# Kernel tuning notes

Measured on AMD Instinct MI355X. Metric: run time of the kernel, lower is better.

## Reference

```python
import jax, jax.numpy as jnp
import numpy as np
import math

B, S, D, H, DFF = 4, 1024, 1024, 16, 4096
DK = D // H
EPS = 1e-5


def setup_inputs() -> dict:
    key = jax.random.key(0)
    ks = jax.random.split(key, 20)
    n = lambda k, shp: jax.random.normal(k, shp, jnp.float32) * 0.02
    inp = {
        "x": jax.random.normal(ks[0], (B, S, D), jnp.float32),
        "enc_output": jax.random.normal(ks[1], (B, S, D), jnp.float32),
        # source_mask is unused by the module's forward; target_mask is causal
        "source_mask": jnp.ones((B, 1, 1, S), jnp.int32),
        "target_mask": jnp.tril(jnp.ones((1, 1, S, S), jnp.int32)),
        # self-attention (torch Linear: y = x @ W.T + b)
        "sa_wq": n(ks[2], (D, D)), "sa_bq": jnp.zeros((D,), jnp.float32),
        "sa_wk": n(ks[3], (D, D)), "sa_bk": jnp.zeros((D,), jnp.float32),
        "sa_wv": n(ks[4], (D, D)), "sa_bv": jnp.zeros((D,), jnp.float32),
        "sa_wo": n(ks[5], (D, D)), "sa_bo": jnp.zeros((D,), jnp.float32),
        # cross-attention (nn.MultiheadAttention packed in_proj)
        "ca_in_w": n(ks[6], (3 * D, D)), "ca_in_b": jnp.zeros((3 * D,), jnp.float32),
        "ca_out_w": n(ks[7], (D, D)), "ca_out_b": jnp.zeros((D,), jnp.float32),
        # feed-forward
        "ff_w1": n(ks[8], (DFF, D)), "ff_b1": jnp.zeros((DFF,), jnp.float32),
        "ff_w2": n(ks[9], (D, DFF)), "ff_b2": jnp.zeros((D,), jnp.float32),
        # layer norms
        "n1_g": jnp.ones((D,), jnp.float32), "n1_b": jnp.zeros((D,), jnp.float32),
        "n2_g": jnp.ones((D,), jnp.float32), "n2_b": jnp.zeros((D,), jnp.float32),
        "n3_g": jnp.ones((D,), jnp.float32), "n3_b": jnp.zeros((D,), jnp.float32),
    }
    return inp


def _layernorm(x, g, b):
    m = jnp.mean(x, axis=-1, keepdims=True)
    v = jnp.var(x, axis=-1, keepdims=True)
    return (x - m) * jax.lax.rsqrt(v + EPS) * g + b


def _split_heads(t):  # [B,L,D] -> [B,H,L,DK]
    Bb, L, _ = t.shape
    return t.reshape(Bb, L, H, DK).transpose(0, 2, 1, 3)


def _attn(q, k, v, mask):
    # q,k,v: [B,H,Lq/ Lk, DK]
    scores = jnp.einsum("bhqd,bhkd->bhqk", q, k) / math.sqrt(DK)
    if mask is not None:
        scores = jnp.where(mask == 0, jnp.float32(-1e9), scores)
    probs = jax.nn.softmax(scores, axis=-1)
    out = jnp.einsum("bhqk,bhkd->bhqd", probs, v)  # [B,H,Lq,DK]
    Bb, _, Lq, _ = out.shape
    return out.transpose(0, 2, 1, 3).reshape(Bb, Lq, D)


def reference(x, enc_output, source_mask, target_mask,
              sa_wq, sa_bq, sa_wk, sa_bk, sa_wv, sa_bv, sa_wo, sa_bo,
              ca_in_w, ca_in_b, ca_out_w, ca_out_b,
              ff_w1, ff_b1, ff_w2, ff_b2,
              n1_g, n1_b, n2_g, n2_b, n3_g, n3_b):
    # --- masked causal self-attention (hand-rolled MultiHeadAttention) ---
    q = _split_heads(x @ sa_wq.T + sa_bq)
    k = _split_heads(x @ sa_wk.T + sa_bk)
    v = _split_heads(x @ sa_wv.T + sa_bv)
    sa = _attn(q, k, v, target_mask) @ sa_wo.T + sa_bo
    x = _layernorm(x + sa, n1_g, n1_b)  # dropout p=0 -> identity

    # --- cross-attention (nn.MultiheadAttention, batch_first, no mask) ---
    wq, wk, wv = ca_in_w[:D], ca_in_w[D:2 * D], ca_in_w[2 * D:]
    bq, bk, bv = ca_in_b[:D], ca_in_b[D:2 * D], ca_in_b[2 * D:]
    q = _split_heads(x @ wq.T + bq)
    k = _split_heads(enc_output @ wk.T + bk)
    v = _split_heads(enc_output @ wv.T + bv)
    ca = _attn(q, k, v, None) @ ca_out_w.T + ca_out_b
    x = _layernorm(x + ca, n2_g, n2_b)

    # --- feed-forward ---
    ff = jax.nn.relu(x @ ff_w1.T + ff_b1) @ ff_w2.T + ff_b2
    x = _layernorm(x + ff, n3_g, n3_b)
    return x
```

## Files before the change

### kernel.cpp

```cpp
#include <hip/hip_runtime.h>
#include <hip/hip_bf16.h>
#include <stdint.h>
#include <math.h>

#define DEV static __device__ __forceinline__

typedef short bf16x8 __attribute__((ext_vector_type(8)));
typedef float f32x4 __attribute__((ext_vector_type(4)));
typedef float f32x16 __attribute__((ext_vector_type(16)));
typedef unsigned short u16;

static constexpr int Sq   = 1024;
static constexpr int Dm   = 1024;
static constexpr int Hh   = 16;
static constexpr int Mrows = 4096;
static constexpr int DFFn = 4096;


DEV u16 f2bf(float f) {
    union { float f; unsigned u; } c; c.f = f;
    unsigned u = c.u;
    return (u16)((u + 0x7FFFu + ((u >> 16) & 1u)) >> 16);
}

DEV float bf2f(u16 v) {
    union { unsigned u; float f; } c; c.u = ((unsigned)v) << 16; return c.f;
}

DEV unsigned cvt_pk_bf16(float lo, float hi) {
    unsigned r;
    asm("v_cvt_pk_bf16_f32 %0, %1, %2" : "=v"(r) : "v"(lo), "v"(hi));
    return r;
}

DEV float fast_exp2(float x) {
#if __has_builtin(__builtin_amdgcn_exp2f)
    return __builtin_amdgcn_exp2f(x);
#else
    float r; asm("v_exp_f32 %0, %1" : "=v"(r) : "v"(x)); return r;
#endif
}

DEV void gload_lds16(void* lds, const void* g) {
    using gvp = __attribute__((address_space(1))) void*;
    using lvp = __attribute__((address_space(3))) void*;
    __builtin_amdgcn_global_load_lds((gvp)const_cast<void*>(g), (lvp)lds, 16, 0, 0);
}

DEV int swz64(int L) { return L ^ (((L >> 7) & 7) << 4); }


__global__ __launch_bounds__(256) void cast_multi_kernel(
    const float* s0, const float* s1, const float* s2, const float* s3, const float* s4,
    const float* s5, const float* s6, const float* s7, const float* s8, const float* s9,
    u16* d0, u16* d1, u16* d2, u16* d3, u16* d4,
    u16* d5, u16* d6, u16* d7, u16* d8, u16* d9,
    int e0, int e1, int e2, int e3, int e4,
    int e5, int e6, int e7, int e8, int e9)
{
    int i = blockIdx.x * 256 + threadIdx.x;
    if (i >= e9) return;
    const float* s; u16* d; int b;
    if      (i < e0) { s = s0; d = d0; b = 0;  }
    else if (i < e1) { s = s1; d = d1; b = e0; }
    else if (i < e2) { s = s2; d = d2; b = e1; }
    else if (i < e3) { s = s3; d = d3; b = e2; }
    else if (i < e4) { s = s4; d = d4; b = e3; }
    else if (i < e5) { s = s5; d = d5; b = e4; }
    else if (i < e6) { s = s6; d = d6; b = e5; }
    else if (i < e7) { s = s7; d = d7; b = e6; }
    else if (i < e8) { s = s8; d = d8; b = e7; }
    else             { s = s9; d = d9; b = e8; }
    int j = i - b;
    float4 v = ((const float4*)s)[j];
    ushort4 o;
    o.x = f2bf(v.x); o.y = f2bf(v.y); o.z = f2bf(v.z); o.w = f2bf(v.w);
    ((ushort4*)d)[j] = o;
}


template<int MODE, int BSPLIT>
__global__ __launch_bounds__(512) void gemm256_kernel(
    const u16* __restrict__ A, const u16* __restrict__ W,
    const float* __restrict__ bias0, const float* __restrict__ bias1,
    const float* __restrict__ bias2,
    void* __restrict__ Cout,
    void* __restrict__ P1, void* __restrict__ P2, void* __restrict__ P3,
    int N, int ldK, int Kpass)
{
    __shared__ char ldsA[65536];
    __shared__ char ldsB[65536];
    const int tid = threadIdx.x;
    const int w = tid >> 6, l = tid & 63;
    const int lr = l & 15, lg = l >> 4;
    const int wr = w >> 2, wc = w & 3;

    const int nwg = gridDim.x * gridDim.y;
    const int lin = blockIdx.y * gridDim.x + blockIdx.x;
    const int swz = (lin & 7) * (nwg >> 3) + (lin >> 3);
    const size_t tm = (size_t)(swz / gridDim.x) * 256;
    const size_t tn = (size_t)(swz % gridDim.x) * 256;
    const size_t kz = (size_t)blockIdx.z * Kpass;

    int offA[8], offB[4];
    #pragma unroll
    for (int m = 0; m < 8; ++m)
        offA[m] = swz64((wr * 128 + m * 16 + lr) * 64 + lg * 16);
    #pragma unroll
    for (int n = 0; n < 4; ++n)
        offB[n] = swz64((wc * 64 + n * 16 + lr) * 64 + lg * 16);

    const int Ls = swz64(tid * 16);
    const int sr = Ls >> 6, scc = Ls & 63;
    const size_t ldb = (size_t)ldK * 2;
    const char* aS = (const char*)A + (tm + sr) * ldb + kz * 2 + scc;
    const char* bS = (const char*)W + (tn + sr) * ldb + kz * 2 + scc;

    auto AH = [&](int b, int h) -> char* { return ldsA + (b * 2 + h) * 16384; };
    auto BH = [&](int b, int h) -> char* { return ldsB + (b * 2 + h) * 16384; };
    auto stage = [&](char* half, const char* src) {
        gload_lds16(half + w * 1024, src);
        gload_lds16(half + 8192 + w * 1024, src + 128 * ldb);
    };

    const int nt = Kpass >> 6;
    const int niter = nt >> 1;

    f32x4 acc[8][4] = {};
    bf16x8 bq[4];

    stage(AH(0, 0), aS);        stage(BH(0, 0), bS);
    stage(AH(0, 1), aS + 64);   stage(BH(0, 1), bS + 64);
    stage(AH(1, 0), aS + 128);  stage(BH(1, 0), bS + 128);
    asm volatile("s_waitcnt vmcnt(4)" ::: "memory");
    __builtin_amdgcn_s_barrier();

    for (int it = 0; it < niter; ++it) {
        const int t0 = it * 2;
        const bool last = (it == niter - 1);
        #pragma unroll
        for (int p = 0; p < 8; ++p) {
            const int ts = p >> 2;
            const int kk = (p >> 1) & 1, mh = p & 1;

            if (mh == 0) {
                #pragma unroll
                for (int n = 0; n < 4; ++n)
                    bq[n] = *(const bf16x8*)(BH(ts, kk) + offB[n]);
            }
            bf16x8 aF[4];
            #pragma unroll
            for (int q = 0; q < 4; ++q)
                aF[q] = *(const bf16x8*)(AH(ts, kk) + offA[mh * 4 + q]);

            if (p == 0)      { stage(AH(1, 1), aS + (size_t)(t0 + 1) * 128 + 64); }
            else if (p == 1) { stage(BH(1, 1), bS + (size_t)(t0 + 1) * 128 + 64); }
            else if (p == 2) { if (t0 + 2 < nt) stage(AH(0, 0), aS + (size_t)(t0 + 2) * 128); }
            else if (p == 3) { if (t0 + 2 < nt) stage(BH(0, 0), bS + (size_t)(t0 + 2) * 128); }
            else if (p == 4) { if (t0 + 2 < nt) stage(AH(0, 1), aS + (size_t)(t0 + 2) * 128 + 64); }
            else if (p == 5) { if (t0 + 2 < nt) stage(BH(0, 1), bS + (size_t)(t0 + 2) * 128 + 64); }
            else if (p == 6) { if (t0 + 3 < nt) stage(AH(1, 0), aS + (size_t)(t0 + 3) * 128); }
            else             { if (t0 + 3 < nt) stage(BH(1, 0), bS + (size_t)(t0 + 3) * 128); }

            if (p == 3) {
                if (last) asm volatile("s_waitcnt vmcnt(0)" ::: "memory");
                else      asm volatile("s_waitcnt vmcnt(4)" ::: "memory");
            } else if (p == 7 && !last) {
                asm volatile("s_waitcnt vmcnt(4)" ::: "memory");
            }
            __builtin_amdgcn_s_barrier();
            asm volatile("s_waitcnt lgkmcnt(0)");
            __builtin_amdgcn_sched_barrier(0);
            __builtin_amdgcn_s_setprio(1);
            #pragma unroll
            for (int q = 0; q < 4; ++q)
                #pragma unroll
                for (int n = 0; n < 4; ++n)
                    acc[mh * 4 + q][n] = __builtin_amdgcn_mfma_f32_16x16x32_bf16(
                        aF[q], bq[n], acc[mh * 4 + q][n], 0, 0, 0);
            __builtin_amdgcn_s_setprio(0);
            __builtin_amdgcn_s_barrier();
        }
    }

    u16* Pp = nullptr;
    float bv[4];
    if (MODE == 3) {
        Pp = (u16*)((blockIdx.z == 0) ? Cout : (blockIdx.z == 1) ? P1 : (blockIdx.z == 2) ? P2 : P3);
    } else {
        #pragma unroll
        for (int n = 0; n < 4; ++n) {
            const int col = (int)tn + wc * 64 + n * 16 + lr;
            if (BSPLIT) {
                const float* bp = (col < 1024) ? bias0 : (col < 2048) ? bias1 : bias2;
                bv[n] = bp[col & 1023];
            } else {
                bv[n] = bias0[col];
            }
        }
    }
    #pragma unroll
    for (int m = 0; m < 8; ++m) {
        #pragma unroll
        for (int n = 0; n < 4; ++n) {
            const size_t col = tn + wc * 64 + n * 16 + lr;
            #pragma unroll
            for (int j = 0; j < 4; ++j) {
                const size_t row = tm + wr * 128 + m * 16 + lg * 4 + j;
                if (MODE == 3) {
                    Pp[row * (size_t)N + col] = f2bf(acc[m][n][j]);
                } else {
                    float v = acc[m][n][j] + bv[n];
                    if (MODE == 2) v = fmaxf(v, 0.f);
                    ((u16*)Cout)[row * (size_t)N + col] = f2bf(v);
                }
            }
        }
    }
}


template<int OUT_BF16, int RELU>
__global__ __launch_bounds__(256) void gemm_bt64_kernel(
    const u16* __restrict__ A, const u16* __restrict__ W,
    const float* __restrict__ bias, void* __restrict__ Cout,
    int N, int K)
{
    __shared__ char Ald[64 * 64];
    __shared__ char Bld[128 * 64];
    const int tid = threadIdx.x;
    const int w  = tid >> 6, l = tid & 63;
    const int lr = l & 15,  lg = l >> 4;

    const int nwg = gridDim.x * gridDim.y;
    const int lin = blockIdx.y * gridDim.x + blockIdx.x;
    const int swz = (lin & 7) * (nwg >> 3) + (lin >> 3);
    const size_t tm = (size_t)(swz / gridDim.x) * 64;
    const size_t tn = (size_t)(swz % gridDim.x) * 128;

    const int Ls = swz64(tid * 16);
    const int sr = Ls >> 6, scc = Ls & 63;
    const u16* Asrc = A + (tm + sr) * (size_t)K + (scc >> 1);
    const u16* Bsrc = W + (tn + sr) * (size_t)K + (scc >> 1);
    char* AldW = Ald + w * 1024;
    char* BldW = Bld + w * 1024;

    f32x4 acc[4][2] = {};

    for (int k0 = 0; k0 < K; k0 += 32) {
        __syncthreads();
        gload_lds16(AldW,        Asrc + k0);
        gload_lds16(BldW,        Bsrc + k0);
        gload_lds16(BldW + 4096, Bsrc + (size_t)64 * K + k0);
        __syncthreads();

        bf16x8 af[4], bfv[2];
        #pragma unroll
        for (int m = 0; m < 4; ++m)
            af[m] = *(const bf16x8*)(Ald + swz64((m * 16 + lr) * 64 + lg * 16));
        #pragma unroll
        for (int n = 0; n < 2; ++n)
            bfv[n] = *(const bf16x8*)(Bld + swz64((w * 32 + n * 16 + lr) * 64 + lg * 16));
        #pragma unroll
        for (int m = 0; m < 4; ++m)
            #pragma unroll
            for (int n = 0; n < 2; ++n)
                acc[m][n] = __builtin_amdgcn_mfma_f32_16x16x32_bf16(af[m], bfv[n], acc[m][n], 0, 0, 0);
    }

    float bv[2];
    #pragma unroll
    for (int n = 0; n < 2; ++n) bv[n] = bias[tn + w * 32 + n * 16 + lr];

    #pragma unroll
    for (int m = 0; m < 4; ++m) {
        #pragma unroll
        for (int n = 0; n < 2; ++n) {
            const size_t col = tn + w * 32 + n * 16 + lr;
            #pragma unroll
            for (int j = 0; j < 4; ++j) {
                const size_t row = tm + m * 16 + lg * 4 + j;
                float v = acc[m][n][j] + bv[n];
                if (RELU) v = fmaxf(v, 0.f);
                if (OUT_BF16) ((u16*)Cout)[row * (size_t)N + col] = f2bf(v);
                else          ((float*)Cout)[row * (size_t)N + col] = v;
            }
        }
    }
}


template<int CAUSAL>
__global__ __launch_bounds__(512, 2) void attn_kernel(
    const u16* __restrict__ Qm, int ldq,
    const u16* __restrict__ Km, int ldk,
    const u16* __restrict__ Vm, int ldv,
    u16* __restrict__ Om)
{
    __shared__ char lds[33280];

    const int tid = threadIdx.x;
    const int w = tid >> 6, l = tid & 63;
    const int lq = l & 31, hi = l >> 5;
    const int s = w & 3, hfk = w >> 2;
    const int bh = blockIdx.x;
    const int b = bh >> 4, h = bh & 15;
    const int q0 = (CAUSAL ? (gridDim.y - 1 - blockIdx.y) : blockIdx.y) * 128;
    const int qw0 = q0 + s * 32;
    const size_t baseQ = (size_t)b * Sq * ldq + (size_t)h * 64;
    const size_t baseK = (size_t)b * Sq * ldk + (size_t)h * 64;
    const size_t baseV = (size_t)b * Sq * ldv + (size_t)h * 64;
    const size_t baseO = (size_t)b * Sq * Dm  + (size_t)h * 64;

    const int qrow = qw0 + lq;
    bf16x8 bq[4];
    #pragma unroll
    for (int kc = 0; kc < 4; ++kc)
        bq[kc] = *(const bf16x8*)&Qm[baseQ + (size_t)qrow * ldq + kc * 16 + hi * 8];

    const int tl = tid & 255, pstg = tid >> 8;
    const int kr  = tl >> 2;
    const int kcB = (tl & 3) * 32;
    const int vdg = tl >> 5;
    const int vkp = tl & 31;
    char* Kst = lds + pstg * 8192;
    char* Vst = lds + 16384 + pstg * 8192;
    const char* Kb_ = lds + hfk * 8192;
    const char* Vb_ = lds + 16384 + hfk * 8192;

    f32x16 o0 = {}, o1 = {};
    float lj = 0.f;

    const int nt_blk  = CAUSAL ? ((q0 + 128) >> 6) : (Sq >> 6);
    const int nrounds = nt_blk >> 1;
    const float cexp = 0.125f * 1.44269504f;
    const float CSH  = 10.0f;

    uint4 kaA, kbA, vaA, vbA, kaB, kbB, vaB, vbB;
    auto loadKV = [&](int rv, uint4& ka, uint4& kb, uint4& va, uint4& vb) {
        const int kv = (rv * 2 + pstg) << 6;
        ka = *(const uint4*)&Km[baseK + (size_t)(kv + kr) * ldk + kcB / 2];
        kb = *(const uint4*)&Km[baseK + (size_t)(kv + kr) * ldk + kcB / 2 + 8];
        va = *(const uint4*)&Vm[baseV + (size_t)(kv + vkp * 2    ) * ldv + vdg * 8];
        vb = *(const uint4*)&Vm[baseV + (size_t)(kv + vkp * 2 + 1) * ldv + vdg * 8];
    };

    loadKV(0, kaA, kbA, vaA, vbA);
    if (nrounds > 1) loadKV(1, kaB, kbB, vaB, vbB);

    for (int r = 0; r < nrounds; ++r) {
        {
            const int sk = (kr & 7) << 4;
            *(uint4*)(Kst + kr * 128 + ((kcB     ) ^ sk)) = kaA;
            *(uint4*)(Kst + kr * 128 + ((kcB + 16) ^ sk)) = kbA;
            const u16* pa_ = (const u16*)&vaA;
            const u16* pb_ = (const u16*)&vbA;
            #pragma unroll
            for (int i = 0; i < 8; ++i) {
                const int d = vdg * 8 + i;
                unsigned val = (unsigned)pa_[i] | ((unsigned)pb_[i] << 16);
                *(unsigned*)(Vst + d * 128 + ((vkp * 4) ^ ((d & 7) << 4))) = val;
            }
        }
        __syncthreads();
        if (r + 2 < nrounds) loadKV(r + 2, kaA, kbA, vaA, vbA);

        const int kv0 = (r * 2 + hfk) << 6;
        if (!CAUSAL || kv0 < qw0 + 32) {
            const int skq = (lq & 7) << 4;

            f32x16 sv[2] = {};
            #pragma unroll
            for (int n = 0; n < 2; ++n) {
                const int rowb = (n * 32 + lq) * 128;
                #pragma unroll
                for (int kc = 0; kc < 4; ++kc) {
                    bf16x8 kf = *(const bf16x8*)(Kb_ + rowb + ((kc * 32 + hi * 16) ^ skq));
                    sv[n] = __builtin_amdgcn_mfma_f32_32x32x16_bf16(kf, bq[kc], sv[n], 0, 0, 0);
                }
            }

            const bool diag = CAUSAL && (kv0 + 63 > qw0);
            float rs0 = 0.f, rs1 = 0.f;
            #pragma unroll
            for (int n = 0; n < 2; ++n)
                #pragma unroll
                for (int r2 = 0; r2 < 16; ++r2) {
                    float v = sv[n][r2];
                    if (diag) {
                        int key = kv0 + n * 32 + (r2 & 3) + 8 * (r2 >> 2) + 4 * hi;
                        if (key > qrow) v = -3.0e8f;
                    }
                    float e = fast_exp2(fmaf(v, cexp, -CSH));
                    sv[n][r2] = e;
                    if (r2 & 1) rs1 += e; else rs0 += e;
                }
            float rs = rs0 + rs1;
            rs += __shfl_xor(rs, 32);
            lj += rs;

            unsigned wv[2][8];
            #pragma unroll
            for (int n = 0; n < 2; ++n)
                #pragma unroll
                for (int m = 0; m < 8; ++m)
                    wv[n][m] = cvt_pk_bf16(sv[n][2 * m], sv[n][2 * m + 1]);

            #pragma unroll
            for (int ks = 0; ks < 4; ++ks) {
                const int n = ks >> 1, q_ = (ks & 1) * 4;
                unsigned r0 = (unsigned)__shfl_xor((int)wv[n][q_ + 0], 32);
                unsigned r1 = (unsigned)__shfl_xor((int)wv[n][q_ + 1], 32);
                unsigned r2w = (unsigned)__shfl_xor((int)wv[n][q_ + 2], 32);
                unsigned r3 = (unsigned)__shfl_xor((int)wv[n][q_ + 3], 32);
                union { unsigned u[4]; bf16x8 v; } pa;
                pa.u[0] = hi ? r2w          : wv[n][q_ + 0];
                pa.u[1] = hi ? r3           : wv[n][q_ + 1];
                pa.u[2] = hi ? wv[n][q_ + 2] : r0;
                pa.u[3] = hi ? wv[n][q_ + 3] : r1;
                const int koff = (ks * 32 + hi * 16);
                bf16x8 vf0 = *(const bf16x8*)(Vb_ + lq * 128        + (koff ^ skq));
                bf16x8 vf1 = *(const bf16x8*)(Vb_ + (32 + lq) * 128 + (koff ^ skq));
                o0 = __builtin_amdgcn_mfma_f32_32x32x16_bf16(pa.v, vf0, o0, 0, 0, 0);
                o1 = __builtin_amdgcn_mfma_f32_32x32x16_bf16(pa.v, vf1, o1, 0, 0, 0);
            }
        }
        __syncthreads();

        uint4 t;
        t = kaA; kaA = kaB; kaB = t;
        t = kbA; kbA = kbB; kbB = t;
        t = vaA; vaA = vaB; vaB = t;
        t = vbA; vbA = vbB; vbB = t;
    }

    char* ob = lds + s * 8192 + l * 128;
    float* mlb = (float*)(lds + 32768) + s * 32 + lq;
    const int sko = (l & 7) << 4;

    if (hfk == 1) {
        #pragma unroll
        for (int i = 0; i < 4; ++i) {
            f32x4 t0v = { o0[4 * i], o0[4 * i + 1], o0[4 * i + 2], o0[4 * i + 3] };
            f32x4 t1v = { o1[4 * i], o1[4 * i + 1], o1[4 * i + 2], o1[4 * i + 3] };
            *(f32x4*)(ob + ((i * 16) ^ sko))      = t0v;
            *(f32x4*)(ob + ((64 + i * 16) ^ sko)) = t1v;
        }
        if (hi == 0) mlb[0] = lj;
    }
    __syncthreads();
    if (hfk == 0) {
        const float linv = __builtin_amdgcn_rcpf(lj + mlb[0]);
        f32x4 b0[4], b1[4];
        #pragma unroll
        for (int i = 0; i < 4; ++i) {
            b0[i] = *(const f32x4*)(ob + ((i * 16) ^ sko));
            b1[i] = *(const f32x4*)(ob + ((64 + i * 16) ^ sko));
        }
        #pragma unroll
        for (int r2 = 0; r2 < 16; ++r2) {
            const int crow = (r2 & 3) + 8 * (r2 >> 2) + 4 * hi;
            const float lr_ = __shfl(linv, crow);
            const size_t rowoff = baseO + (size_t)(qw0 + crow) * Dm;
            float v0 = (o0[r2] + b0[r2 >> 2][r2 & 3]) * lr_;
            float v1 = (o1[r2] + b1[r2 >> 2][r2 & 3]) * lr_;
            Om[rowoff + lq]      = f2bf(v0);
            Om[rowoff + 32 + lq] = f2bf(v1);
        }
    }
}


__global__ __launch_bounds__(256) void add_ln_kernel(
    const float* __restrict__ A, const float* __restrict__ Bv,
    const float* __restrict__ g, const float* __restrict__ be,
    float* __restrict__ Y, u16* __restrict__ Ybf)
{
    const int row = blockIdx.x;
    const int tid = threadIdx.x;
    const size_t off = (size_t)row * Dm;
    float4 a4 = ((const float4*)(A + off))[tid];
    float4 b4 = ((const float4*)(Bv + off))[tid];
    float4 xv;
    xv.x = a4.x + b4.x; xv.y = a4.y + b4.y; xv.z = a4.z + b4.z; xv.w = a4.w + b4.w;
    float s = xv.x + xv.y + xv.z + xv.w;
    float q = xv.x * xv.x + xv.y * xv.y + xv.z * xv.z + xv.w * xv.w;
    #pragma unroll
    for (int m = 1; m < 64; m <<= 1) {
        s += __shfl_xor(s, m);
        q += __shfl_xor(q, m);
    }
    __shared__ float ss[4], qq[4];
    if ((tid & 63) == 0) { ss[tid >> 6] = s; qq[tid >> 6] = q; }
    __syncthreads();
    s = ss[0] + ss[1] + ss[2] + ss[3];
    q = qq[0] + qq[1] + qq[2] + qq[3];
    const float mean = s * (1.f / 1024.f);
    const float var  = q * (1.f / 1024.f) - mean * mean;
    const float rstd = rsqrtf(var + 1e-5f);
    float4 g4  = ((const float4*)g)[tid];
    float4 be4 = ((const float4*)be)[tid];
    float4 y;
    y.x = (xv.x - mean) * rstd * g4.x + be4.x;
    y.y = (xv.y - mean) * rstd * g4.y + be4.y;
    y.z = (xv.z - mean) * rstd * g4.z + be4.z;
    y.w = (xv.w - mean) * rstd * g4.w + be4.w;
    ((float4*)(Y + off))[tid] = y;
    if (Ybf) {
        ushort4 ob;
        ob.x = f2bf(y.x); ob.y = f2bf(y.y); ob.z = f2bf(y.z); ob.w = f2bf(y.w);
        ((ushort4*)(Ybf + off))[tid] = ob;
    }
}


__global__ __launch_bounds__(256) void add_ln_red4_kernel(
    const float* __restrict__ X,
    const u16* __restrict__ P0, const u16* __restrict__ P1,
    const u16* __restrict__ P2, const u16* __restrict__ P3,
    const float* __restrict__ bias,
    const float* __restrict__ g, const float* __restrict__ be,
    float* __restrict__ Y)
{
    const int row = blockIdx.x;
    const int tid = threadIdx.x;
    const size_t off = (size_t)row * Dm;
    float4 a4 = ((const float4*)(X + off))[tid];
    ushort4 u0 = ((const ushort4*)(P0 + off))[tid];
    ushort4 u1 = ((const ushort4*)(P1 + off))[tid];
    ushort4 u2 = ((const ushort4*)(P2 + off))[tid];
    ushort4 u3 = ((const ushort4*)(P3 + off))[tid];
    float4 b4 = ((const float4*)bias)[tid];
    float4 xv;
    xv.x = a4.x + bf2f(u0.x) + bf2f(u1.x) + bf2f(u2.x) + bf2f(u3.x) + b4.x;
    xv.y = a4.y + bf2f(u0.y) + bf2f(u1.y) + bf2f(u2.y) + bf2f(u3.y) + b4.y;
    xv.z = a4.z + bf2f(u0.z) + bf2f(u1.z) + bf2f(u2.z) + bf2f(u3.z) + b4.z;
    xv.w = a4.w + bf2f(u0.w) + bf2f(u1.w) + bf2f(u2.w) + bf2f(u3.w) + b4.w;
    float s = xv.x + xv.y + xv.z + xv.w;
    float q = xv.x * xv.x + xv.y * xv.y + xv.z * xv.z + xv.w * xv.w;
    #pragma unroll
    for (int m = 1; m < 64; m <<= 1) {
        s += __shfl_xor(s, m);
        q += __shfl_xor(q, m);
    }
    __shared__ float ss[4], qq[4];
    if ((tid & 63) == 0) { ss[tid >> 6] = s; qq[tid >> 6] = q; }
    __syncthreads();
    s = ss[0] + ss[1] + ss[2] + ss[3];
    q = qq[0] + qq[1] + qq[2] + qq[3];
    const float mean = s * (1.f / 1024.f);
    const float var  = q * (1.f / 1024.f) - mean * mean;
    const float rstd = rsqrtf(var + 1e-5f);
    float4 g4  = ((const float4*)g)[tid];
    float4 be4 = ((const float4*)be)[tid];
    float4 y;
    y.x = (xv.x - mean) * rstd * g4.x + be4.x;
    y.y = (xv.y - mean) * rstd * g4.y + be4.y;
    y.z = (xv.z - mean) * rstd * g4.z + be4.z;
    y.w = (xv.w - mean) * rstd * g4.w + be4.w;
    ((float4*)(Y + off))[tid] = y;
}


extern "C" void kernel_launch(void* const* d_in, const int* in_sizes, int n_in,
                              void* d_out, int out_size, void* d_ws, size_t ws_size,
                              hipStream_t stream)
{
    const float* x       = (const float*)d_in[0];
    const float* enc     = (const float*)d_in[1];
    const float* sa_wq   = (const float*)d_in[4];
    const float* sa_bq   = (const float*)d_in[5];
    const float* sa_wk   = (const float*)d_in[6];
    const float* sa_bk   = (const float*)d_in[7];
    const float* sa_wv   = (const float*)d_in[8];
    const float* sa_bv   = (const float*)d_in[9];
    const float* sa_wo   = (const float*)d_in[10];
    const float* sa_bo   = (const float*)d_in[11];
    const float* ca_in_w = (const float*)d_in[12];
    const float* ca_in_b = (const float*)d_in[13];
    const float* ca_out_w= (const float*)d_in[14];
    const float* ca_out_b= (const float*)d_in[15];
    const float* ff_w1   = (const float*)d_in[16];
    const float* ff_b1   = (const float*)d_in[17];
    const float* ff_w2   = (const float*)d_in[18];
    const float* ff_b2   = (const float*)d_in[19];
    const float* n1_g = (const float*)d_in[20];
    const float* n1_b = (const float*)d_in[21];
    const float* n2_g = (const float*)d_in[22];
    const float* n2_b = (const float*)d_in[23];
    const float* n3_g = (const float*)d_in[24];
    const float* n3_b = (const float*)d_in[25];

    char* p = (char*)d_ws;
    auto take = [&](size_t bytes) -> char* {
        char* r = p; p += (bytes + 255) & ~(size_t)255; return r;
    };
    const size_t MDbf = (size_t)Mrows * Dm * 2;
    const size_t MDf  = (size_t)Mrows * Dm * 4;
    const size_t DD   = (size_t)Dm * Dm;

    u16* xb     = (u16*)take(MDbf);
    u16* encb   = (u16*)take(MDbf);
    u16* wqkv   = (u16*)take(3 * DD * 2);
    u16* wob    = (u16*)take(DD * 2);
    u16* cainb  = (u16*)take(3 * DD * 2);
    u16* caoutb = (u16*)take(DD * 2);
    u16* fw1b   = (u16*)take((size_t)DFFn * Dm * 2);
    u16* fw2b   = (u16*)take((size_t)Dm * DFFn * 2);
    u16* SCR    = (u16*)take((size_t)Mrows * DFFn * 2);
    u16* AOb    = (u16*)take(MDbf);
    float* tmpf = (float*)take(MDf);
    float* x1f  = (float*)take(MDf);
    u16*   x1b  = (u16*)take(MDbf);
    float* x2f  = (float*)take(MDf);
    u16*   x2b  = (u16*)take(MDbf);
    if ((size_t)(p - (char*)d_ws) > ws_size) return;

    u16* fp0 = AOb;
    u16* fp1 = (u16*)tmpf;
    u16* fp2 = (u16*)tmpf + 4 * 1024 * 1024;
    u16* fp3 = xb;

    {
        const int sx  = (int)((size_t)Mrows * Dm / 4);
        const int sw  = (int)(DD / 4);
        const int e0 = sx;
        const int e1 = e0 + sx;
        const int e2 = e1 + sw;
        const int e3 = e2 + sw;
        const int e4 = e3 + sw;
        const int e5 = e4 + sw;
        const int e6 = e5 + 3 * sw;
        const int e7 = e6 + sw;
        const int e8 = e7 + 4 * sw;
        const int e9 = e8 + 4 * sw;
        cast_multi_kernel<<<dim3((e9 + 255) / 256), dim3(256), 0, stream>>>(
            x, enc, sa_wq, sa_wk, sa_wv, sa_wo, ca_in_w, ca_out_w, ff_w1, ff_w2,
            xb, encb, wqkv, wqkv + DD, wqkv + 2 * DD, wob, cainb, caoutb, fw1b, fw2b,
            e0, e1, e2, e3, e4, e5, e6, e7, e8, e9);
    }

    const dim3 blk(256);
    const dim3 blk512(512);
    const size_t M4 = (size_t)Mrows * Dm;

    gemm256_kernel<1, 1><<<dim3(12, 16), blk512, 0, stream>>>(
        xb, wqkv, sa_bq, sa_bk, sa_bv, (void*)SCR, nullptr, nullptr, nullptr, 3072, Dm, Dm);
    attn_kernel<1><<<dim3(4 * Hh, Sq / 128), blk512, 0, stream>>>(SCR, 3072, SCR + 1024, 3072, SCR + 2048, 3072, AOb);
    gemm_bt64_kernel<0, 0><<<dim3(Dm / 128, Mrows / 64), blk, 0, stream>>>(AOb, wob, sa_bo, (void*)tmpf, Dm, Dm);
    add_ln_kernel<<<dim3(Mrows), blk, 0, stream>>>(x, tmpf, n1_g, n1_b, x1f, x1b);

    u16* Qc  = SCR;
    u16* KVc = SCR + M4;
    gemm_bt64_kernel<1, 0><<<dim3(Dm / 128, Mrows / 64), blk, 0, stream>>>(x1b, cainb, ca_in_b, (void*)Qc, Dm, Dm);
    gemm256_kernel<1, 1><<<dim3(8, 16), blk512, 0, stream>>>(
        encb, cainb + DD, ca_in_b + Dm, ca_in_b + 2 * Dm, ca_in_b + 2 * Dm,
        (void*)KVc, nullptr, nullptr, nullptr, 2048, Dm, Dm);
    attn_kernel<0><<<dim3(4 * Hh, Sq / 128), blk512, 0, stream>>>(Qc, 1024, KVc, 2048, KVc + 1024, 2048, AOb);
    gemm_bt64_kernel<0, 0><<<dim3(Dm / 128, Mrows / 64), blk, 0, stream>>>(AOb, caoutb, ca_out_b, (void*)tmpf, Dm, Dm);
    add_ln_kernel<<<dim3(Mrows), blk, 0, stream>>>(x1f, tmpf, n2_g, n2_b, x2f, x2b);

    u16* ffh = SCR;
    gemm256_kernel<2, 0><<<dim3(16, 16), blk512, 0, stream>>>(
        x2b, fw1b, ff_b1, ff_b1, ff_b1, (void*)ffh, nullptr, nullptr, nullptr, DFFn, Dm, Dm);
    gemm256_kernel<3, 0><<<dim3(4, 16, 4), blk512, 0, stream>>>(
        ffh, fw2b, nullptr, nullptr, nullptr, (void*)fp0, (void*)fp1, (void*)fp2, (void*)fp3, Dm, DFFn, 1024);
    add_ln_red4_kernel<<<dim3(Mrows), blk, 0, stream>>>(x2f, fp0, fp1, fp2, fp3, ff_b2, n3_g, n3_b, (float*)d_out);
}
```

Before: 325.8 us.

## Double-buffer LDS tiles in 64-wide GEMM and drop extra barrier in main GEMM

Rewrites the small-tile GEMM to use double-buffered LDS with a BK of 64, prefetching the next K-tile while MFMAs run on the current one. This replaces the per-step load-then-sync pattern and cuts the barrier count per K-step. It also adds an occupancy hint to the launch bounds and removes a trailing s_barrier in the large GEMM's phase loop. The barrier removal risks an LDS race if that barrier was guarding buffer reuse.

```diff
diff --git a/kernel.cpp b/kernel.cpp
--- a/kernel.cpp
+++ b/kernel.cpp
@@ -179,7 +179,6 @@
                     acc[mh * 4 + q][n] = __builtin_amdgcn_mfma_f32_16x16x32_bf16(
                         aF[q], bq[n], acc[mh * 4 + q][n], 0, 0, 0);
             __builtin_amdgcn_s_setprio(0);
-            __builtin_amdgcn_s_barrier();
         }
     }
 
@@ -221,13 +220,13 @@
 
 
 template<int OUT_BF16, int RELU>
-__global__ __launch_bounds__(256) void gemm_bt64_kernel(
+__global__ __launch_bounds__(256, 3) void gemm_bt64_kernel(
     const u16* __restrict__ A, const u16* __restrict__ W,
     const float* __restrict__ bias, void* __restrict__ Cout,
     int N, int K)
 {
-    __shared__ char Ald[64 * 64];
-    __shared__ char Bld[128 * 64];
+    __shared__ char Ald[2][8192];
+    __shared__ char Bld[2][16384];
     const int tid = threadIdx.x;
     const int w  = tid >> 6, l = tid & 63;
     const int lr = l & 15,  lg = l >> 4;
@@ -239,33 +238,61 @@
     const size_t tn = (size_t)(swz % gridDim.x) * 128;
 
     const int Ls = swz64(tid * 16);
-    const int sr = Ls >> 6, scc = Ls & 63;
-    const u16* Asrc = A + (tm + sr) * (size_t)K + (scc >> 1);
-    const u16* Bsrc = W + (tn + sr) * (size_t)K + (scc >> 1);
-    char* AldW = Ald + w * 1024;
-    char* BldW = Bld + w * 1024;
+    const int sr = Ls >> 7, sc = (Ls & 127) >> 1;
+    const u16* As = A + (tm + sr) * (size_t)K + sc;
+    const u16* Bs = W + (tn + sr) * (size_t)K + sc;
+    const int woff = w * 1024;
+
+    auto stage = [&](int b, int k0) {
+        gload_lds16(Ald[b] + woff,         As + k0);
+        gload_lds16(Ald[b] + 4096 + woff,  As + (size_t)32 * K + k0);
+        gload_lds16(Bld[b] + woff,         Bs + k0);
+        gload_lds16(Bld[b] + 4096 + woff,  Bs + (size_t)32 * K + k0);
+        gload_lds16(Bld[b] + 8192 + woff,  Bs + (size_t)64 * K + k0);
+        gload_lds16(Bld[b] + 12288 + woff, Bs + (size_t)96 * K + k0);
+    };
+
+    int offA[4][2], offB[2][2];
+    #pragma unroll
+    for (int m = 0; m < 4; ++m)
+        #pragma unroll
+        for (int kk = 0; kk < 2; ++kk)
+            offA[m][kk] = swz64((m * 16 + lr) * 128 + kk * 64 + lg * 16);
+    #pragma unroll
+    for (int n = 0; n < 2; ++n)
+        #pragma unroll
+        for (int kk = 0; kk < 2; ++kk)
+            offB[n][kk] = swz64((w * 32 + n * 16 + lr) * 128 + kk * 64 + lg * 16);
 
     f32x4 acc[4][2] = {};
-
-    for (int k0 = 0; k0 < K; k0 += 32) {
+    const int nt = K >> 6;
+
+    stage(0, 0);
+    asm volatile("s_waitcnt vmcnt(0)" ::: "memory");
+    __syncthreads();
+
+    for (int t = 0; t < nt; ++t) {
+        const int cur = t & 1;
+        if (t + 1 < nt) stage(cur ^ 1, (t + 1) * 64);
+        #pragma unroll
+        for (int kk = 0; kk < 2; ++kk) {
+            bf16x8 aF[4], bq[2];
+            #pragma unroll
+            for (int m = 0; m < 4; ++m) aF[m] = *(const bf16x8*)(Ald[cur] + offA[m][kk]);
+            #pragma unroll
+            for (int n = 0; n < 2; ++n) bq[n] = *(const bf16x8*)(Bld[cur] + offB[n][kk]);
+            asm volatile("s_waitcnt lgkmcnt(0)");
+            __builtin_amdgcn_sched_barrier(0);
+            __builtin_amdgcn_s_setprio(1);
+            #pragma unroll
+            for (int m = 0; m < 4; ++m)
+                #pragma unroll
+                for (int n = 0; n < 2; ++n)
+                    acc[m][n] = __builtin_amdgcn_mfma_f32_16x16x32_bf16(aF[m], bq[n], acc[m][n], 0, 0, 0);
+            __builtin_amdgcn_s_setprio(0);
+        }
+        if (t + 1 < nt) asm volatile("s_waitcnt vmcnt(0)" ::: "memory");
         __syncthreads();
-        gload_lds16(AldW,        Asrc + k0);
-        gload_lds16(BldW,        Bsrc + k0);
-        gload_lds16(BldW + 4096, Bsrc + (size_t)64 * K + k0);
-        __syncthreads();
-
-        bf16x8 af[4], bfv[2];
-        #pragma unroll
-        for (int m = 0; m < 4; ++m)
-            af[m] = *(const bf16x8*)(Ald + swz64((m * 16 + lr) * 64 + lg * 16));
-        #pragma unroll
-        for (int n = 0; n < 2; ++n)
-            bfv[n] = *(const bf16x8*)(Bld + swz64((w * 32 + n * 16 + lr) * 64 + lg * 16));
-        #pragma unroll
-        for (int m = 0; m < 4; ++m)
-            #pragma unroll
-            for (int n = 0; n < 2; ++n)
-                acc[m][n] = __builtin_amdgcn_mfma_f32_16x16x32_bf16(af[m], bfv[n], acc[m][n], 0, 0, 0);
     }
 
     float bv[2];
```

Result: faster. 305.4 us (-6.3%).
